# Kernel optimization log

Measured on AMD Instinct MI355X. Metric: run time of the kernel, lower is better.

The kernel has to match this reference:

```python
import jax, jax.numpy as jnp
import numpy as np

B, S, C, HD = 2, 4096, 2048, 128
H = C // HD  # 16 heads
EPS = 1.1920929e-07  # torch RMSNorm default eps for float32 (finfo.eps)


def _make_rope(seq_len, head_dim):
    # Standard RoPE 2x2 rotation matrices: [1, S, 1, head_dim//2, 2, 2]
    half = head_dim // 2
    freqs = 1.0 / (10000.0 ** (np.arange(0, half, dtype=np.float32) / half))
    ang = np.arange(seq_len, dtype=np.float32)[:, None] * freqs[None, :]  # [S, half]
    cos, sin = np.cos(ang), np.sin(ang)
    rot = np.stack([np.stack([cos, -sin], axis=-1),
                    np.stack([sin, cos], axis=-1)], axis=-2)  # [S, half, 2, 2]
    return jnp.asarray(rot[None, :, None])  # [1, S, 1, half, 2, 2]


def setup_inputs() -> dict:
    key = jax.random.key(0)
    ks = jax.random.split(key, 9)
    sc = 1.0 / np.sqrt(C)
    return {
        "x": jax.random.normal(ks[0], (B, S, C), jnp.float32),
        "rope": _make_rope(S, HD),
        "wq": jax.random.normal(ks[1], (C, C), jnp.float32) * sc,
        "bq": jax.random.normal(ks[2], (C,), jnp.float32) * 0.01,
        "wk": jax.random.normal(ks[3], (C, C), jnp.float32) * sc,
        "bk": jax.random.normal(ks[4], (C,), jnp.float32) * 0.01,
        "wv": jax.random.normal(ks[5], (C, C), jnp.float32) * sc,
        "bv": jax.random.normal(ks[6], (C,), jnp.float32) * 0.01,
        "q_norm_w": jnp.ones((HD,), jnp.float32),
        "k_norm_w": jnp.ones((HD,), jnp.float32),
    }


def _rmsnorm(t, w):
    t32 = t.astype(jnp.float32)
    inv = jax.lax.rsqrt(jnp.mean(t32 * t32, axis=-1, keepdims=True) + EPS)
    return (t32 * inv * w).astype(t.dtype)


def _apply_rotary(t, rope):
    # t: [B, S, H, HD] -> pairs [B, S, H, HD//2, 1, 2]; rope: [1, S, 1, HD//2, 2, 2]
    t32 = t.reshape(*t.shape[:-1], HD // 2, 1, 2).astype(jnp.float32)
    out = (rope * t32).sum(axis=-1)  # [B, S, H, HD//2, 2]
    return out.reshape(t.shape).astype(t.dtype)


def reference(x, rope, wq, bq, wk, bk, wv, bv, q_norm_w, k_norm_w):
    # QKV projections (torch Linear: x @ W^T + b)
    q = (jnp.einsum('bsc,oc->bso', x, wq) + bq).reshape(B, S, H, HD)
    k = (jnp.einsum('bsc,oc->bso', x, wk) + bk).reshape(B, S, H, HD)
    v = (jnp.einsum('bsc,oc->bso', x, wv) + bv).reshape(B, S, H, HD)
    # Per-head RMSNorm on q, k (in float32, cast back), then rotary
    q = _apply_rotary(_rmsnorm(q, q_norm_w), rope)
    k = _apply_rotary(_rmsnorm(k, k_norm_w), rope)
    return (q, k, v)
```

## Files before the change

kernel.cpp:

```cpp
#include <hip/hip_runtime.h>


#define M_DIM 8192
#define N_DIM 6144
#define K_DIM 2048
#define NKT 32
#define EPS_RMS 1.1920929e-07f

typedef __bf16 bf16x8 __attribute__((ext_vector_type(8)));
typedef float f32x4 __attribute__((ext_vector_type(4)));

__device__ __forceinline__ void gload16(const void* g, void* l) {
  __builtin_amdgcn_global_load_lds(
      (const __attribute__((address_space(1))) unsigned int*)g,
      (__attribute__((address_space(3))) unsigned int*)l, 16, 0, 0);
}

__device__ __forceinline__ unsigned ldsoff(const void* p) {
  return (unsigned)(unsigned long long)(const __attribute__((address_space(3))) char*)p;
}

__device__ __forceinline__ unsigned short f2bf(float f) {
  union { float f; unsigned u; } x; x.f = f;
  unsigned r = x.u + 0x7FFFu + ((x.u >> 16) & 1u);
  return (unsigned short)(r >> 16);
}

__global__ void __launch_bounds__(256) cvt_kernel(const float* __restrict__ s,
                                                  unsigned short* __restrict__ d, int n4) {
  int i = blockIdx.x * blockDim.x + threadIdx.x;
  const int stride = gridDim.x * blockDim.x;
  for (; i < n4; i += stride) {
    const float4 v = reinterpret_cast<const float4*>(s)[i];
    ushort4 o;
    o.x = f2bf(v.x); o.y = f2bf(v.y); o.z = f2bf(v.z); o.w = f2bf(v.w);
    reinterpret_cast<ushort4*>(d)[i] = o;
  }
}

#define DSR(dst, base, IMM) \
  asm volatile("ds_read_b128 %0, %1 offset:" IMM : "=v"(dst) : "v"(base))

#define MFMA_PH(MH, NH)                                                              \
  {                                                                                  \
    _Pragma("unroll")                                                                \
    for (int mf4 = 0; mf4 < 4; ++mf4) {                                              \
      _Pragma("unroll")                                                              \
      for (int nf2 = 0; nf2 < 2; ++nf2) {                                            \
        f32x4& c = acc[(MH) * 4 + mf4][(NH) * 2 + nf2];                              \
        c = __builtin_amdgcn_mfma_f32_16x16x32_bf16(                                 \
            __builtin_bit_cast(bf16x8, Af[mf4][0]),                                  \
            __builtin_bit_cast(bf16x8, Bf[NH][nf2][0]), c, 0, 0, 0);                 \
        c = __builtin_amdgcn_mfma_f32_16x16x32_bf16(                                 \
            __builtin_bit_cast(bf16x8, Af[mf4][1]),                                  \
            __builtin_bit_cast(bf16x8, Bf[NH][nf2][1]), c, 0, 0, 0);                 \
      }                                                                              \
    }                                                                                \
  }

__global__ void __launch_bounds__(512, 2) gemm_fused(
    const unsigned short* __restrict__ xbf, const unsigned short* __restrict__ wbf,
    const float* __restrict__ rope,
    const float* __restrict__ bq, const float* __restrict__ bk, const float* __restrict__ bv,
    const float* __restrict__ qnw, const float* __restrict__ knw,
    float* __restrict__ dout) {
  const int id = blockIdx.x;
  const int sw = (id & 7) * 96 + (id >> 3);
  const int bm = sw / 24;
  const int bn = sw - bm * 24;
  const int m0 = bm << 8, n0 = bn << 8;
  const int tid = threadIdx.x;
  const int w = tid >> 6, l = tid & 63;
  const int l15 = l & 15, lhi = l >> 4;
  const int wr = w >> 2, wc = w & 3;

  __shared__ __align__(16) unsigned short As[32768];
  __shared__ __align__(16) unsigned short Bs[32768];

  const int srow = tid >> 3;
  const int schunk = (tid & 7) ^ (srow & 7);
  const unsigned short* aSrc = xbf + ((size_t)(m0 + srow) << 11) + (schunk << 3);
  const unsigned short* bSrc = wbf + ((size_t)(n0 + srow) << 11) + (schunk << 3);
  char* aDst = (char*)As + (w << 10);
  char* bDst = (char*)Bs + (w << 10);

#define STA(KT, Q) gload16(aSrc + ((size_t)(Q) << 17) + ((KT) << 6), aDst + ((((KT) & 1) << 15) + ((Q) << 13)))
#define STB(KT, Q) gload16(bSrc + ((size_t)(Q) << 17) + ((KT) << 6), bDst + ((((KT) & 1) << 15) + ((Q) << 13)))

  const int sl0 = ((lhi ^ (l15 & 7)) << 4);
  const int sl1 = (((lhi + 4) ^ (l15 & 7)) << 4);
  unsigned a0 = ldsoff(As) + (wr << 14) + (l15 << 7) + sl0;
  unsigned a1 = ldsoff(As) + (wr << 14) + (l15 << 7) + sl1;
  unsigned b0 = ldsoff(Bs) + (wc << 13) + (l15 << 7) + sl0;
  unsigned b1 = ldsoff(Bs) + (wc << 13) + (l15 << 7) + sl1;

  f32x4 acc[8][4];
#pragma unroll
  for (int i = 0; i < 8; ++i)
#pragma unroll
    for (int j = 0; j < 4; ++j) acc[i][j] = (f32x4){0.f, 0.f, 0.f, 0.f};

  f32x4 Af[4][2];
  f32x4 Bf[2][2][2];

  STA(0, 0); STA(0, 2);
  STB(0, 0); STB(0, 1); STB(0, 2); STB(0, 3);
  STA(0, 1); STA(0, 3);
  asm volatile("s_waitcnt vmcnt(2)");
  __builtin_amdgcn_s_barrier();

  for (int kt = 0; kt < NKT; ++kt) {
    const bool notLast = (kt < NKT - 1);
    DSR(Af[0][0], a0, "0");    DSR(Af[1][0], a0, "2048");
    DSR(Af[2][0], a0, "4096"); DSR(Af[3][0], a0, "6144");
    DSR(Af[0][1], a1, "0");    DSR(Af[1][1], a1, "2048");
    DSR(Af[2][1], a1, "4096"); DSR(Af[3][1], a1, "6144");
    DSR(Bf[0][0][0], b0, "0");    DSR(Bf[0][1][0], b0, "2048");
    DSR(Bf[0][0][1], b1, "0");    DSR(Bf[0][1][1], b1, "2048");
    if (notLast) { STA(kt + 1, 0); STA(kt + 1, 2); STB(kt + 1, 0); STB(kt + 1, 1); }
    __builtin_amdgcn_s_barrier();
    asm volatile("s_waitcnt lgkmcnt(0)");
    __builtin_amdgcn_sched_barrier(0);
    __builtin_amdgcn_s_setprio(1);
    MFMA_PH(0, 0);
    __builtin_amdgcn_s_setprio(0);
    __builtin_amdgcn_s_barrier();
    DSR(Bf[1][0][0], b0, "4096"); DSR(Bf[1][1][0], b0, "6144");
    DSR(Bf[1][0][1], b1, "4096"); DSR(Bf[1][1][1], b1, "6144");
    if (notLast) { STB(kt + 1, 2); STB(kt + 1, 3); }
    __builtin_amdgcn_s_barrier();
    asm volatile("s_waitcnt lgkmcnt(0)");
    __builtin_amdgcn_sched_barrier(0);
    __builtin_amdgcn_s_setprio(1);
    MFMA_PH(0, 1);
    __builtin_amdgcn_s_setprio(0);
    if (notLast) { asm volatile("s_waitcnt vmcnt(6)"); }
    else         { asm volatile("s_waitcnt vmcnt(0)"); }
    __builtin_amdgcn_s_barrier();
    DSR(Af[0][0], a0, "8192");  DSR(Af[1][0], a0, "10240");
    DSR(Af[2][0], a0, "12288"); DSR(Af[3][0], a0, "14336");
    DSR(Af[0][1], a1, "8192");  DSR(Af[1][1], a1, "10240");
    DSR(Af[2][1], a1, "12288"); DSR(Af[3][1], a1, "14336");
    if (notLast) { STA(kt + 1, 1); STA(kt + 1, 3); }
    __builtin_amdgcn_s_barrier();
    asm volatile("s_waitcnt lgkmcnt(0)");
    __builtin_amdgcn_sched_barrier(0);
    __builtin_amdgcn_s_setprio(1);
    MFMA_PH(1, 1);
    MFMA_PH(1, 0);
    __builtin_amdgcn_s_setprio(0);
    if (notLast) { asm volatile("s_waitcnt vmcnt(2)"); }
    __builtin_amdgcn_s_barrier();
    a0 ^= 32768u; a1 ^= 32768u; b0 ^= 32768u; b1 ^= 32768u;
  }

  float* scr = (float*)As;
  const int sec = bn >> 3;
  const int nsec = (n0 & 2047) + (wc << 6);
  const float* bias = sec == 0 ? bq : (sec == 1 ? bk : bv);
  float biasv[4];
#pragma unroll
  for (int nf = 0; nf < 4; ++nf) biasv[nf] = bias[nsec + nf * 16 + l15];
  const size_t outBase = ((size_t)sec << 24);

  if (sec < 2) {
    const float* nwp = sec ? knw : qnw;
    const int colh = (wc & 1) << 6;
    float nwv[4];
#pragma unroll
    for (int nf = 0; nf < 4; ++nf) nwv[nf] = nwp[colh + nf * 16 + l15];
    float ssv[8][4];
#pragma unroll
    for (int mf = 0; mf < 8; ++mf) {
#pragma unroll
      for (int j = 0; j < 4; ++j) {
        float ss = 0.f;
#pragma unroll
        for (int nf = 0; nf < 4; ++nf) {
          const float t = acc[mf][nf][j] + biasv[nf];
          ss += t * t;
        }
        ss += __shfl_xor(ss, 1);
        ss += __shfl_xor(ss, 2);
        ss += __shfl_xor(ss, 4);
        ss += __shfl_xor(ss, 8);
        ssv[mf][j] = ss;
      }
    }
    if (l15 == 0) {
#pragma unroll
      for (int mf = 0; mf < 8; ++mf)
#pragma unroll
        for (int j = 0; j < 4; ++j)
          scr[(w << 7) + mf * 16 + (lhi << 2) + j] = ssv[mf][j];
    }
    __syncthreads();
#pragma unroll
    for (int mf = 0; mf < 8; ++mf) {
#pragma unroll
      for (int j = 0; j < 4; ++j) {
        const float tot = ssv[mf][j] + scr[((w ^ 1) << 7) + mf * 16 + (lhi << 2) + j];
        const float inv = rsqrtf(tot * (1.0f / 128.0f) + EPS_RMS);
        const int m = m0 + (wr << 7) + mf * 16 + (lhi << 2) + j;
        const float* rp = rope + ((size_t)(m & 4095) << 8);
        float* orow = dout + outBase + ((size_t)m << 11) + nsec + l15;
#pragma unroll
        for (int nf = 0; nf < 4; ++nf) {
          const float tn = (acc[mf][nf][j] + biasv[nf]) * inv * nwv[nf];
          const float pn = __shfl_xor(tn, 1);
          const int ch = colh + nf * 16 + l15;
          const int jr = ch >> 1;
          const float o = fmaf(rp[jr << 2], tn, rp[(jr << 2) + 1 + (ch & 1)] * pn);
          orow[nf << 4] = o;
        }
      }
    }
  } else {
#pragma unroll
    for (int mf = 0; mf < 8; ++mf)
#pragma unroll
      for (int j = 0; j < 4; ++j) {
        const int m = m0 + (wr << 7) + mf * 16 + (lhi << 2) + j;
        float* orow = dout + outBase + ((size_t)m << 11) + nsec + l15;
#pragma unroll
        for (int nf = 0; nf < 4; ++nf) orow[nf << 4] = acc[mf][nf][j] + biasv[nf];
      }
  }
}

extern "C" void kernel_launch(void* const* d_in, const int* in_sizes, int n_in,
                              void* d_out, int out_size, void* d_ws, size_t ws_size,
                              hipStream_t stream) {
  const float* x = (const float*)d_in[0];
  const float* rope = (const float*)d_in[1];
  const float* wq = (const float*)d_in[2];
  const float* bq = (const float*)d_in[3];
  const float* wk = (const float*)d_in[4];
  const float* bk = (const float*)d_in[5];
  const float* wv = (const float*)d_in[6];
  const float* bv = (const float*)d_in[7];
  const float* qnw = (const float*)d_in[8];
  const float* knw = (const float*)d_in[9];

  unsigned short* xbf = (unsigned short*)d_ws;
  unsigned short* wbf = xbf + (size_t)M_DIM * K_DIM;

  cvt_kernel<<<2048, 256, 0, stream>>>(x, xbf, M_DIM * K_DIM / 4);
  cvt_kernel<<<1024, 256, 0, stream>>>(wq, wbf, K_DIM * K_DIM / 4);
  cvt_kernel<<<1024, 256, 0, stream>>>(wk, wbf + (size_t)K_DIM * K_DIM, K_DIM * K_DIM / 4);
  cvt_kernel<<<1024, 256, 0, stream>>>(wv, wbf + (size_t)2 * K_DIM * K_DIM, K_DIM * K_DIM / 4);

  gemm_fused<<<(M_DIM / 256) * (N_DIM / 256), 512, 0, stream>>>(
      xbf, wbf, rope, bq, bk, bv, qnw, knw, (float*)d_out);
}
```

Before: 265.2 us.

## Replace inline-asm LDS reads with C loads and collapse K-loop barrier phases

Swaps the hand-written ds_read_b128 inline asm and manual lgkmcnt waits for plain C vector loads from shared memory, so the compiler can schedule the reads and insert its own waits. It also merges the first two MFMA phases, loading every B fragment up front and issuing all six B prefetches together, which cuts the per-iteration barrier count from six to two. The intent is to reduce synchronization stalls and let the compiler interleave LDS reads with MFMAs. In exchange it holds more fragment registers live at once, and the compiler may insert conservative waits or schedule loads worse than the hand-tuned sequence.

```diff
diff --git a/kernel.cpp b/kernel.cpp
--- a/kernel.cpp
+++ b/kernel.cpp
@@ -14,10 +14,6 @@
   __builtin_amdgcn_global_load_lds(
       (const __attribute__((address_space(1))) unsigned int*)g,
       (__attribute__((address_space(3))) unsigned int*)l, 16, 0, 0);
-}
-
-__device__ __forceinline__ unsigned ldsoff(const void* p) {
-  return (unsigned)(unsigned long long)(const __attribute__((address_space(3))) char*)p;
 }
 
 __device__ __forceinline__ unsigned short f2bf(float f) {
@@ -38,8 +34,7 @@
   }
 }
 
-#define DSR(dst, base, IMM) \
-  asm volatile("ds_read_b128 %0, %1 offset:" IMM : "=v"(dst) : "v"(base))
+#define LDS4(ARR, BASE, OFF) (*(const f32x4*)((const char*)(ARR) + (BASE) + (OFF)))
 
 #define MFMA_PH(MH, NH)                                                              \
   {                                                                                  \
@@ -89,10 +84,10 @@
 
   const int sl0 = ((lhi ^ (l15 & 7)) << 4);
   const int sl1 = (((lhi + 4) ^ (l15 & 7)) << 4);
-  unsigned a0 = ldsoff(As) + (wr << 14) + (l15 << 7) + sl0;
-  unsigned a1 = ldsoff(As) + (wr << 14) + (l15 << 7) + sl1;
-  unsigned b0 = ldsoff(Bs) + (wc << 13) + (l15 << 7) + sl0;
-  unsigned b1 = ldsoff(Bs) + (wc << 13) + (l15 << 7) + sl1;
+  unsigned a0 = (wr << 14) + (l15 << 7) + sl0;
+  unsigned a1 = (wr << 14) + (l15 << 7) + sl1;
+  unsigned b0 = (wc << 13) + (l15 << 7) + sl0;
+  unsigned b1 = (wc << 13) + (l15 << 7) + sl1;
 
   f32x4 acc[8][4];
 #pragma unroll
@@ -106,51 +101,44 @@
   STA(0, 0); STA(0, 2);
   STB(0, 0); STB(0, 1); STB(0, 2); STB(0, 3);
   STA(0, 1); STA(0, 3);
-  asm volatile("s_waitcnt vmcnt(2)");
+  asm volatile("s_waitcnt vmcnt(2)" ::: "memory");
   __builtin_amdgcn_s_barrier();
+  asm volatile("" ::: "memory");
 
   for (int kt = 0; kt < NKT; ++kt) {
     const bool notLast = (kt < NKT - 1);
-    DSR(Af[0][0], a0, "0");    DSR(Af[1][0], a0, "2048");
-    DSR(Af[2][0], a0, "4096"); DSR(Af[3][0], a0, "6144");
-    DSR(Af[0][1], a1, "0");    DSR(Af[1][1], a1, "2048");
-    DSR(Af[2][1], a1, "4096"); DSR(Af[3][1], a1, "6144");
-    DSR(Bf[0][0][0], b0, "0");    DSR(Bf[0][1][0], b0, "2048");
-    DSR(Bf[0][0][1], b1, "0");    DSR(Bf[0][1][1], b1, "2048");
-    if (notLast) { STA(kt + 1, 0); STA(kt + 1, 2); STB(kt + 1, 0); STB(kt + 1, 1); }
-    __builtin_amdgcn_s_barrier();
-    asm volatile("s_waitcnt lgkmcnt(0)");
-    __builtin_amdgcn_sched_barrier(0);
+    Af[0][0] = LDS4(As, a0, 0);    Af[1][0] = LDS4(As, a0, 2048);
+    Af[2][0] = LDS4(As, a0, 4096); Af[3][0] = LDS4(As, a0, 6144);
+    Af[0][1] = LDS4(As, a1, 0);    Af[1][1] = LDS4(As, a1, 2048);
+    Af[2][1] = LDS4(As, a1, 4096); Af[3][1] = LDS4(As, a1, 6144);
+    Bf[0][0][0] = LDS4(Bs, b0, 0);    Bf[0][1][0] = LDS4(Bs, b0, 2048);
+    Bf[0][0][1] = LDS4(Bs, b1, 0);    Bf[0][1][1] = LDS4(Bs, b1, 2048);
+    Bf[1][0][0] = LDS4(Bs, b0, 4096); Bf[1][1][0] = LDS4(Bs, b0, 6144);
+    Bf[1][0][1] = LDS4(Bs, b1, 4096); Bf[1][1][1] = LDS4(Bs, b1, 6144);
+    if (notLast) {
+      STA(kt + 1, 0); STA(kt + 1, 2);
+      STB(kt + 1, 0); STB(kt + 1, 1); STB(kt + 1, 2); STB(kt + 1, 3);
+    }
     __builtin_amdgcn_s_setprio(1);
     MFMA_PH(0, 0);
-    __builtin_amdgcn_s_setprio(0);
-    __builtin_amdgcn_s_barrier();
-    DSR(Bf[1][0][0], b0, "4096"); DSR(Bf[1][1][0], b0, "6144");
-    DSR(Bf[1][0][1], b1, "4096"); DSR(Bf[1][1][1], b1, "6144");
-    if (notLast) { STB(kt + 1, 2); STB(kt + 1, 3); }
-    __builtin_amdgcn_s_barrier();
-    asm volatile("s_waitcnt lgkmcnt(0)");
-    __builtin_amdgcn_sched_barrier(0);
-    __builtin_amdgcn_s_setprio(1);
     MFMA_PH(0, 1);
     __builtin_amdgcn_s_setprio(0);
-    if (notLast) { asm volatile("s_waitcnt vmcnt(6)"); }
-    else         { asm volatile("s_waitcnt vmcnt(0)"); }
+    if (notLast) { asm volatile("s_waitcnt vmcnt(6)" ::: "memory"); }
+    else         { asm volatile("s_waitcnt vmcnt(0)" ::: "memory"); }
     __builtin_amdgcn_s_barrier();
-    DSR(Af[0][0], a0, "8192");  DSR(Af[1][0], a0, "10240");
-    DSR(Af[2][0], a0, "12288"); DSR(Af[3][0], a0, "14336");
-    DSR(Af[0][1], a1, "8192");  DSR(Af[1][1], a1, "10240");
-    DSR(Af[2][1], a1, "12288"); DSR(Af[3][1], a1, "14336");
+    asm volatile("" ::: "memory");
+    Af[0][0] = LDS4(As, a0, 8192);  Af[1][0] = LDS4(As, a0, 10240);
+    Af[2][0] = LDS4(As, a0, 12288); Af[3][0] = LDS4(As, a0, 14336);
+    Af[0][1] = LDS4(As, a1, 8192);  Af[1][1] = LDS4(As, a1, 10240);
+    Af[2][1] = LDS4(As, a1, 12288); Af[3][1] = LDS4(As, a1, 14336);
     if (notLast) { STA(kt + 1, 1); STA(kt + 1, 3); }
+    __builtin_amdgcn_s_setprio(1);
+    MFMA_PH(1, 0);
+    MFMA_PH(1, 1);
+    __builtin_amdgcn_s_setprio(0);
+    if (notLast) { asm volatile("s_waitcnt vmcnt(2)" ::: "memory"); }
     __builtin_amdgcn_s_barrier();
-    asm volatile("s_waitcnt lgkmcnt(0)");
-    __builtin_amdgcn_sched_barrier(0);
-    __builtin_amdgcn_s_setprio(1);
-    MFMA_PH(1, 1);
-    MFMA_PH(1, 0);
-    __builtin_amdgcn_s_setprio(0);
-    if (notLast) { asm volatile("s_waitcnt vmcnt(2)"); }
-    __builtin_amdgcn_s_barrier();
+    asm volatile("" ::: "memory");
     a0 ^= 32768u; a1 ^= 32768u; b0 ^= 32768u; b1 ^= 32768u;
   }
 
```

Measured after the change: 261.2 us. No clear change (-1.5%).
